# Kernel optimization log

Hardware: AMD Instinct MI355X
Metric: run time of the kernel (lower is better)

The kernel has to match this reference:

```python
import jax, jax.numpy as jnp
import numpy as np

SHIFT = 1  # original module picks random(+1/-1) at init; fixed to +1 for determinism


def setup_inputs() -> dict:
    key = jax.random.key(0)
    k1, k2, k3 = jax.random.split(key, 3)
    x = jax.random.normal(k1, (1024, 1792, 14), dtype=jnp.float32)
    w1 = jax.random.normal(k2, (256, 2), dtype=jnp.float32)      # weights[0]
    w2 = jax.random.normal(k3, (128, 3, 256), dtype=jnp.float32)  # weights[1]
    return {"x": x, "w1": w1, "w2": w2}


def reference(x, w1, w2):
    m = 1024
    # Channels 1792 split as j(128) * l(14); H = 14. unfold((3,1), pad=(1,0)) is an
    # im2col over H with 3 taps; torch orders the unfolded channel dim as c*3+k,
    # so reshape (1024, 128, 14, 3, 14) puts taps k before spatial n -> permute to mjlnk.
    x4 = x.reshape(m, 128, 14, 14)                       # (m, j, l, h)
    xp = jnp.pad(x4, ((0, 0), (0, 0), (0, 0), (1, 1)))   # pad H by 1 each side
    win = jnp.stack([xp[..., 0:14], xp[..., 1:15], xp[..., 2:16]], axis=-1)  # (m,j,l,n,k)
    t4 = jnp.einsum('mjlnk,jki->mlni', win, w2)          # (1024, 14, 14, 256)
    t5 = jnp.einsum('mabj,ji->mabji', t4, w1)            # (1024, 14, 14, 256, 2) outer product
    t6 = jnp.roll(t5, SHIFT, axis=1)
    t6 = t6.transpose(0, 2, 3, 1, 4).reshape(m, 14, 256, 28)
    t6 = jnp.roll(t6, SHIFT, axis=3)
    t6 = t6.reshape(m, 14, 256, 14, 2).sum(axis=4)       # pairwise sum
    return t6.transpose(0, 2, 3, 1)                      # (1024, 256, 14, 14)
```

## Files before the change

### kernel.cpp

```cpp
#include <hip/hip_runtime.h>

typedef __bf16 bf16x8 __attribute__((ext_vector_type(8)));
typedef unsigned short u16x8 __attribute__((ext_vector_type(8)));
typedef float f32x4 __attribute__((ext_vector_type(4)));

__device__ __forceinline__ unsigned short f2bf(float f) {
    unsigned u = __builtin_bit_cast(unsigned, f);
    u += 0x7FFFu + ((u >> 16) & 1u);
    return (unsigned short)(u >> 16);
}
__device__ __forceinline__ float bflo(unsigned w) {
    return __builtin_bit_cast(float, w << 16);
}
__device__ __forceinline__ float bfhi(unsigned w) {
    return __builtin_bit_cast(float, w & 0xFFFF0000u);
}

__global__ void prep_w2(const float* __restrict__ w2, unsigned short* __restrict__ w2t) {
    int idx = blockIdx.x * 256 + threadIdx.x;
    if (idx < 128 * 3 * 256) {
        int i  = idx % 256;
        int jk = idx / 256;
        int j2 = jk / 3, k = jk % 3;
        w2t[i * 384 + k * 128 + j2] = f2bf(w2[idx]);
    }
}

__device__ __forceinline__ void load14(const float* __restrict__ p, bool odd, float v[14]) {
    if (odd) {
        const float2 a  = *(const float2*)(p);
        const float4 q0 = *(const float4*)(p + 2);
        const float4 q1 = *(const float4*)(p + 6);
        const float4 q2 = *(const float4*)(p + 10);
        v[0]=a.x;  v[1]=a.y;
        v[2]=q0.x; v[3]=q0.y; v[4]=q0.z;  v[5]=q0.w;
        v[6]=q1.x; v[7]=q1.y; v[8]=q1.z;  v[9]=q1.w;
        v[10]=q2.x; v[11]=q2.y; v[12]=q2.z; v[13]=q2.w;
    } else {
        const float4 q0 = *(const float4*)(p);
        const float4 q1 = *(const float4*)(p + 4);
        const float4 q2 = *(const float4*)(p + 8);
        const float2 a  = *(const float2*)(p + 12);
        v[0]=q0.x; v[1]=q0.y; v[2]=q0.z;  v[3]=q0.w;
        v[4]=q1.x; v[5]=q1.y; v[6]=q1.z;  v[7]=q1.w;
        v[8]=q2.x; v[9]=q2.y; v[10]=q2.z; v[11]=q2.w;
        v[12]=a.x; v[13]=a.y;
    }
}

__global__ __launch_bounds__(256, 3) void fused_conv_outer2(
    const float* __restrict__ x, const float* __restrict__ w1,
    const unsigned short* __restrict__ w2t, float* __restrict__ out)
{
    __shared__ alignas(16) unsigned short xlds[112 * 136];
    __shared__ alignas(16) unsigned short cb[4 * 112 * 18];

    const int m    = blockIdx.x >> 1;
    const int half = blockIdx.x & 1;
    const int tid  = threadIdx.x;
    const int wave = tid >> 6;
    const int lane = tid & 63;
    const int c16  = lane & 15;
    const int kgrp = lane >> 4;

    {
        const float* xm = x + (size_t)m * 25088;
        const int j2a = 2 * lane;
#pragma unroll
        for (int t = 0; t < 2; ++t) {
            const int li = wave * 2 + t;
            const int gl = half ? (6 + li) : (li < 7 ? li : 13);
            float va[14], vb[14];
            const float* b0 = xm + (size_t)j2a * 196 + gl * 14;
            load14(b0,       (gl & 1) != 0, va);
            load14(b0 + 196, (gl & 1) != 0, vb);
            unsigned short* dst = &xlds[(li * 14) * 136 + j2a];
#pragma unroll
            for (int h = 0; h < 14; ++h) {
                unsigned pk = (unsigned)f2bf(va[h]) | ((unsigned)f2bf(vb[h]) << 16);
                *(unsigned*)&dst[h * 136] = pk;
            }
        }
    }
    __syncthreads();

    unsigned short* cbw = &cb[wave * (112 * 18)];
    float* outm = out + (size_t)m * 50176;

#pragma unroll 1
    for (int nt = 0; nt < 4; ++nt) {
        const int ntile   = wave * 4 + nt;
        const int colbase = ntile * 16;

        bf16x8 Bf[12];
        {
            const unsigned short* bp = w2t + (size_t)(colbase + c16) * 384 + kgrp * 8;
#pragma unroll
            for (int k = 0; k < 12; ++k)
                Bf[k] = __builtin_bit_cast(bf16x8, *(const u16x8*)(bp + k * 32));
        }

#pragma unroll 1
        for (int mt = 0; mt < 7; ++mt) {
            const int r0 = mt * 16 + c16;
            const int nn = r0 % 14;

            bf16x8 Af[12];
#pragma unroll
            for (int k = 0; k < 12; ++k) {
                const int tap = k >> 2;
                const int h   = nn + tap - 1;
                if ((unsigned)h < 14u) {
                    Af[k] = __builtin_bit_cast(bf16x8,
                        *(const u16x8*)&xlds[(r0 + tap - 1) * 136 + (k & 3) * 32 + kgrp * 8]);
                } else {
                    Af[k] = __builtin_bit_cast(bf16x8, (u16x8)(unsigned short)0);
                }
            }

            f32x4 acc = {0.f, 0.f, 0.f, 0.f};
#pragma unroll
            for (int k = 0; k < 12; ++k)
                acc = __builtin_amdgcn_mfma_f32_16x16x32_bf16(Af[k], Bf[k], acc, 0, 0, 0);

            const int rrb = mt * 16 + kgrp * 4;
#pragma unroll
            for (int j = 0; j < 4; ++j)
                cbw[(rrb + j) * 18 + c16] = f2bf(acc[j]);
        }

        asm volatile("s_waitcnt lgkmcnt(0)" ::: "memory");

        float4 wv[8];
#pragma unroll
        for (int cp = 0; cp < 8; ++cp)
            wv[cp] = *(const float4*)(w1 + (colbase + 2 * cp) * 2);

        float* op = outm + (size_t)colbase * 196;
#pragma unroll
        for (int it = 0; it < 2; ++it) {
            const int e   = it * 64 + lane;
            const bool ok = (e < 98);
            const int ec  = ok ? e : 97;
            const int ci  = ec / 14;
            const int n2  = ec - ci * 14;
            int li1, li2, o;
            if (half) { li1 = ci + 1; li2 = ci;            o = e + 112 - (ci == 6 ? 196 : 0); }
            else      { li1 = ci;     li2 = (ci + 7) & 7;  o = e + 14; }
            const int r1o = (li1 * 14 + n2) * 18;
            const int r2o = (li2 * 14 + n2) * 18;
#pragma unroll
            for (int cp = 0; cp < 8; ++cp) {
                const unsigned A = *(const unsigned*)&cbw[r1o + 2 * cp];
                const unsigned B = *(const unsigned*)&cbw[r2o + 2 * cp];
                if (ok) {
                    op[(2 * cp) * 196 + o]     = wv[cp].x * bflo(A) + wv[cp].y * bflo(B);
                    op[(2 * cp + 1) * 196 + o] = wv[cp].z * bfhi(A) + wv[cp].w * bfhi(B);
                }
            }
        }

        asm volatile("" ::: "memory");
    }
}

extern "C" void kernel_launch(void* const* d_in, const int* in_sizes, int n_in,
                              void* d_out, int out_size, void* d_ws, size_t ws_size,
                              hipStream_t stream) {
    const float* x  = (const float*)d_in[0];
    const float* w1 = (const float*)d_in[1];
    const float* w2 = (const float*)d_in[2];
    float* out = (float*)d_out;
    unsigned short* w2t = (unsigned short*)d_ws;

    prep_w2<<<384, 256, 0, stream>>>(w2, w2t);
    fused_conv_outer2<<<2048, 256, 0, stream>>>(x, w1, w2t, out);
}
```

Measured before the change: 361.9 us.

## Pad LDS rows with zero halos and compute two column tiles per A fragment

The x tile in LDS gets explicit zero halo rows per spatial line, so A-fragment loads need no boundary branch. Each wave now processes 32 output columns per pass, reusing one set of A fragments for two MFMA chains and halving the A LDS reads per output. The price is more registers (two B fragment sets), a larger staging buffer, and launch bounds lowered from 3 to 2 blocks per SM. The w1 loads move into the epilogue loop.

```diff
diff --git a/kernel.cpp b/kernel.cpp
--- a/kernel.cpp
+++ b/kernel.cpp
@@ -48,12 +48,12 @@
     }
 }
 
-__global__ __launch_bounds__(256, 3) void fused_conv_outer2(
+__global__ __launch_bounds__(256, 2) void fused_conv_outer3(
     const float* __restrict__ x, const float* __restrict__ w1,
     const unsigned short* __restrict__ w2t, float* __restrict__ out)
 {
-    __shared__ alignas(16) unsigned short xlds[112 * 136];
-    __shared__ alignas(16) unsigned short cb[4 * 112 * 18];
+    __shared__ alignas(16) unsigned short xlds[128 * 136];
+    __shared__ alignas(16) unsigned short cb[4 * 112 * 34];
 
     const int m    = blockIdx.x >> 1;
     const int half = blockIdx.x & 1;
@@ -62,6 +62,13 @@
     const int lane = tid & 63;
     const int c16  = lane & 15;
     const int kgrp = lane >> 4;
+
+    for (int i = tid; i < 1088; i += 256) {
+        const int zr   = i / 68;
+        const int w    = i - zr * 68;
+        const int lrow = (zr >> 1) * 16 + ((zr & 1) ? 15 : 0);
+        *(unsigned*)&xlds[lrow * 136 + w * 2] = 0;
+    }
 
     {
         const float* xm = x + (size_t)m * 25088;
@@ -74,7 +81,7 @@
             const float* b0 = xm + (size_t)j2a * 196 + gl * 14;
             load14(b0,       (gl & 1) != 0, va);
             load14(b0 + 196, (gl & 1) != 0, vb);
-            unsigned short* dst = &xlds[(li * 14) * 136 + j2a];
+            unsigned short* dst = &xlds[(li * 16 + 1) * 136 + j2a];
 #pragma unroll
             for (int h = 0; h < 14; ++h) {
                 unsigned pk = (unsigned)f2bf(va[h]) | ((unsigned)f2bf(vb[h]) << 16);
@@ -84,57 +91,55 @@
     }
     __syncthreads();
 
-    unsigned short* cbw = &cb[wave * (112 * 18)];
+    unsigned short* cbw = &cb[wave * (112 * 34)];
     float* outm = out + (size_t)m * 50176;
 
 #pragma unroll 1
-    for (int nt = 0; nt < 4; ++nt) {
-        const int ntile   = wave * 4 + nt;
-        const int colbase = ntile * 16;
+    for (int np = 0; np < 2; ++np) {
+        const int colbase = wave * 64 + np * 32;
 
-        bf16x8 Bf[12];
+        bf16x8 B0[12], B1[12];
         {
-            const unsigned short* bp = w2t + (size_t)(colbase + c16) * 384 + kgrp * 8;
+            const unsigned short* bp0 = w2t + (size_t)(colbase + c16) * 384 + kgrp * 8;
+            const unsigned short* bp1 = bp0 + 16 * 384;
 #pragma unroll
-            for (int k = 0; k < 12; ++k)
-                Bf[k] = __builtin_bit_cast(bf16x8, *(const u16x8*)(bp + k * 32));
+            for (int k = 0; k < 12; ++k) {
+                B0[k] = __builtin_bit_cast(bf16x8, *(const u16x8*)(bp0 + k * 32));
+                B1[k] = __builtin_bit_cast(bf16x8, *(const u16x8*)(bp1 + k * 32));
+            }
         }
 
 #pragma unroll 1
         for (int mt = 0; mt < 7; ++mt) {
             const int r0 = mt * 16 + c16;
-            const int nn = r0 % 14;
+            const int li = r0 / 14;
+            const int rb = r0 + 2 * li;
 
             bf16x8 Af[12];
 #pragma unroll
             for (int k = 0; k < 12; ++k) {
                 const int tap = k >> 2;
-                const int h   = nn + tap - 1;
-                if ((unsigned)h < 14u) {
-                    Af[k] = __builtin_bit_cast(bf16x8,
-                        *(const u16x8*)&xlds[(r0 + tap - 1) * 136 + (k & 3) * 32 + kgrp * 8]);
-                } else {
-                    Af[k] = __builtin_bit_cast(bf16x8, (u16x8)(unsigned short)0);
-                }
+                Af[k] = __builtin_bit_cast(bf16x8,
+                    *(const u16x8*)&xlds[(rb + tap) * 136 + (k & 3) * 32 + kgrp * 8]);
             }
 
-            f32x4 acc = {0.f, 0.f, 0.f, 0.f};
+            f32x4 a0 = {0.f, 0.f, 0.f, 0.f};
+            f32x4 a1 = {0.f, 0.f, 0.f, 0.f};
 #pragma unroll
-            for (int k = 0; k < 12; ++k)
-                acc = __builtin_amdgcn_mfma_f32_16x16x32_bf16(Af[k], Bf[k], acc, 0, 0, 0);
+            for (int k = 0; k < 12; ++k) {
+                a0 = __builtin_amdgcn_mfma_f32_16x16x32_bf16(Af[k], B0[k], a0, 0, 0, 0);
+                a1 = __builtin_amdgcn_mfma_f32_16x16x32_bf16(Af[k], B1[k], a1, 0, 0, 0);
+            }
 
             const int rrb = mt * 16 + kgrp * 4;
 #pragma unroll
-            for (int j = 0; j < 4; ++j)
-                cbw[(rrb + j) * 18 + c16] = f2bf(acc[j]);
+            for (int j = 0; j < 4; ++j) {
+                cbw[(rrb + j) * 34 + c16]      = f2bf(a0[j]);
+                cbw[(rrb + j) * 34 + 16 + c16] = f2bf(a1[j]);
+            }
         }
 
         asm volatile("s_waitcnt lgkmcnt(0)" ::: "memory");
-
-        float4 wv[8];
-#pragma unroll
-        for (int cp = 0; cp < 8; ++cp)
-            wv[cp] = *(const float4*)(w1 + (colbase + 2 * cp) * 2);
 
         float* op = outm + (size_t)colbase * 196;
 #pragma unroll
@@ -147,15 +152,16 @@
             int li1, li2, o;
             if (half) { li1 = ci + 1; li2 = ci;            o = e + 112 - (ci == 6 ? 196 : 0); }
             else      { li1 = ci;     li2 = (ci + 7) & 7;  o = e + 14; }
-            const int r1o = (li1 * 14 + n2) * 18;
-            const int r2o = (li2 * 14 + n2) * 18;
+            const int r1o = (li1 * 14 + n2) * 34;
+            const int r2o = (li2 * 14 + n2) * 34;
 #pragma unroll
-            for (int cp = 0; cp < 8; ++cp) {
+            for (int cp = 0; cp < 16; ++cp) {
+                const float4 wv = *(const float4*)(w1 + (colbase + 2 * cp) * 2);
                 const unsigned A = *(const unsigned*)&cbw[r1o + 2 * cp];
                 const unsigned B = *(const unsigned*)&cbw[r2o + 2 * cp];
                 if (ok) {
-                    op[(2 * cp) * 196 + o]     = wv[cp].x * bflo(A) + wv[cp].y * bflo(B);
-                    op[(2 * cp + 1) * 196 + o] = wv[cp].z * bfhi(A) + wv[cp].w * bfhi(B);
+                    op[(2 * cp) * 196 + o]     = wv.x * bflo(A) + wv.y * bflo(B);
+                    op[(2 * cp + 1) * 196 + o] = wv.z * bfhi(A) + wv.w * bfhi(B);
                 }
             }
         }
@@ -174,5 +180,5 @@
     unsigned short* w2t = (unsigned short*)d_ws;
 
     prep_w2<<<384, 256, 0, stream>>>(w2, w2t);
-    fused_conv_outer2<<<2048, 256, 0, stream>>>(x, w1, w2t, out);
+    fused_conv_outer3<<<2048, 256, 0, stream>>>(x, w1, w2t, out);
 }
```

New measurement: 368.1 us. Within noise of the previous version (+1.7%).
